# Performance work log

Hardware: AMD Instinct MI355X
Metric: run time of the kernel (lower is better)

The kernel has to match this reference:

```python
import jax, jax.numpy as jnp
import numpy as np

B = 4194304  # batch of 3x3 rotation matrices


def _make_rotations(key, b):
    k1, k2 = jax.random.split(key)
    axis = jax.random.normal(k1, (b, 3), dtype=jnp.float32)
    axis = axis / jnp.linalg.norm(axis, axis=1, keepdims=True)
    # angles bounded away from 0 and pi (s_theta = 2*sin(theta) must be nonzero)
    theta = jax.random.uniform(k2, (b,), dtype=jnp.float32, minval=0.1, maxval=np.pi - 0.1)
    x, y, z = axis[:, 0], axis[:, 1], axis[:, 2]
    zero = jnp.zeros_like(x)
    K = jnp.stack([zero, -z, y, z, zero, -x, -y, x, zero], axis=1).reshape(b, 3, 3)
    I = jnp.eye(3, dtype=jnp.float32)
    s = jnp.sin(theta)[:, None, None]
    c = jnp.cos(theta)[:, None, None]
    return I + s * K + (1.0 - c) * (K @ K)  # Rodrigues


def setup_inputs() -> dict:
    key = jax.random.key(0)
    return {"mat_batch": _make_rotations(key, B)}


def reference(mat_batch) -> jnp.ndarray:
    # rotation angle from trace: theta = acos((tr(R) - 1) / 2)
    tr = jnp.trace(mat_batch, axis1=1, axis2=2)  # [B]
    rot_angle = jnp.arccos((tr - 1.0) / 2.0)[:, None]  # [B,1]
    s_theta = 2.0 * jnp.sin(rot_angle)  # [B,1]
    # unnormalized axis from skew-symmetric part
    w = jnp.stack(
        [
            mat_batch[:, 2, 1] - mat_batch[:, 1, 2],
            mat_batch[:, 0, 2] - mat_batch[:, 2, 0],
            mat_batch[:, 1, 0] - mat_batch[:, 0, 1],
        ],
        axis=1,
    )  # [B,3]
    rot_axis = w / s_theta
    return rot_angle * rot_axis  # [B,3] twist = theta * axis
```

## Files before the change

kernel.cpp:

```cpp
#include <hip/hip_runtime.h>
#include <math.h>


__global__ __launch_bounds__(256) void mat2twist_kernel(
    const float4* __restrict__ in4,
    float4* __restrict__ out4,
    int n_quads,
    const float* __restrict__ in_s,
    float* __restrict__ out_s,
    int n_mat) {

    int idx = blockIdx.x * blockDim.x + threadIdx.x;
    int stride = gridDim.x * blockDim.x;

    for (int q = idx; q < n_quads; q += stride) {
        const float4* p = in4 + (size_t)q * 9;
        float m[36];
#pragma unroll
        for (int i = 0; i < 9; ++i) {
            float4 v = p[i];
            m[4 * i + 0] = v.x;
            m[4 * i + 1] = v.y;
            m[4 * i + 2] = v.z;
            m[4 * i + 3] = v.w;
        }
        float r[12];
#pragma unroll
        for (int j = 0; j < 4; ++j) {
            const float* a = m + 9 * j;
            float tr = a[0] + a[4] + a[8];
            float c  = 0.5f * (tr - 1.0f);
            float ang = acosf(c);
            float s2 = fmaxf(1.0f - c * c, 1e-30f);
            float k  = ang * 0.5f / sqrtf(s2);
            r[3 * j + 0] = k * (a[7] - a[5]);
            r[3 * j + 1] = k * (a[2] - a[6]);
            r[3 * j + 2] = k * (a[3] - a[1]);
        }
        float4* o = out4 + (size_t)q * 3;
        o[0] = make_float4(r[0], r[1], r[2],  r[3]);
        o[1] = make_float4(r[4], r[5], r[6],  r[7]);
        o[2] = make_float4(r[8], r[9], r[10], r[11]);
    }

    if (idx == 0) {
        for (int i = n_quads * 4; i < n_mat; ++i) {
            const float* a = in_s + (size_t)i * 9;
            float tr = a[0] + a[4] + a[8];
            float c  = 0.5f * (tr - 1.0f);
            float ang = acosf(c);
            float s2 = fmaxf(1.0f - c * c, 1e-30f);
            float k  = ang * 0.5f / sqrtf(s2);
            out_s[3 * i + 0] = k * (a[7] - a[5]);
            out_s[3 * i + 1] = k * (a[2] - a[6]);
            out_s[3 * i + 2] = k * (a[3] - a[1]);
        }
    }
}

extern "C" void kernel_launch(void* const* d_in, const int* in_sizes, int n_in,
                              void* d_out, int out_size, void* d_ws, size_t ws_size,
                              hipStream_t stream) {
    const float* in = (const float*)d_in[0];
    float* out = (float*)d_out;
    int n_mat = in_sizes[0] / 9;
    int n_quads = n_mat / 4;

    int block = 256;
    int grid = (n_quads + block - 1) / block;
    if (grid > 4096) grid = 4096;
    if (grid < 1) grid = 1;

    mat2twist_kernel<<<grid, block, 0, stream>>>(
        (const float4*)in, (float4*)out, n_quads, in, out, n_mat);
}
```

Baseline: 223.8 us.

## Stage matrix loads and twist stores through LDS for coalesced global access

Result: no change. 225.5 us (+0.8%).

```diff
diff --git a/kernel.cpp b/kernel.cpp
--- a/kernel.cpp
+++ b/kernel.cpp
@@ -2,7 +2,7 @@
 #include <math.h>
 
 
-__global__ __launch_bounds__(256) void mat2twist_kernel(
+__global__ __launch_bounds__(256) void mat2twist_lds_kernel(
     const float4* __restrict__ in4,
     float4* __restrict__ out4,
     int n_quads,
@@ -10,47 +10,62 @@
     float* __restrict__ out_s,
     int n_mat) {
 
-    int idx = blockIdx.x * blockDim.x + threadIdx.x;
-    int stride = gridDim.x * blockDim.x;
+    __shared__ float4 lds[256 * 9];
 
-    for (int q = idx; q < n_quads; q += stride) {
-        const float4* p = in4 + (size_t)q * 9;
-        float m[36];
+    const int t = threadIdx.x;
+
+    for (int qbase = blockIdx.x * 256; qbase < n_quads; qbase += gridDim.x * 256) {
+        const int quads_here = min(256, n_quads - qbase);
+        const int in_total4  = quads_here * 9;
+
+        const float4* src = in4 + (size_t)qbase * 9;
+        for (int i = t; i < in_total4; i += 256) {
+            lds[i] = src[i];
+        }
+        __syncthreads();
+
+        float r[12];
+        const bool active = t < quads_here;
+        if (active) {
+            const float* m = (const float*)(lds + t * 9);
 #pragma unroll
-        for (int i = 0; i < 9; ++i) {
-            float4 v = p[i];
-            m[4 * i + 0] = v.x;
-            m[4 * i + 1] = v.y;
-            m[4 * i + 2] = v.z;
-            m[4 * i + 3] = v.w;
+            for (int j = 0; j < 4; ++j) {
+                const float* a = m + 9 * j;
+                float tr  = a[0] + a[4] + a[8];
+                float c   = 0.5f * (tr - 1.0f);
+                float ang = acosf(c);
+                float s2  = fmaxf(1.0f - c * c, 1e-30f);
+                float k   = ang * 0.5f / sqrtf(s2);
+                r[3 * j + 0] = k * (a[7] - a[5]);
+                r[3 * j + 1] = k * (a[2] - a[6]);
+                r[3 * j + 2] = k * (a[3] - a[1]);
+            }
         }
-        float r[12];
-#pragma unroll
-        for (int j = 0; j < 4; ++j) {
-            const float* a = m + 9 * j;
-            float tr = a[0] + a[4] + a[8];
-            float c  = 0.5f * (tr - 1.0f);
-            float ang = acosf(c);
-            float s2 = fmaxf(1.0f - c * c, 1e-30f);
-            float k  = ang * 0.5f / sqrtf(s2);
-            r[3 * j + 0] = k * (a[7] - a[5]);
-            r[3 * j + 1] = k * (a[2] - a[6]);
-            r[3 * j + 2] = k * (a[3] - a[1]);
+        __syncthreads();
+
+        if (active) {
+            lds[t * 3 + 0] = make_float4(r[0], r[1], r[2],  r[3]);
+            lds[t * 3 + 1] = make_float4(r[4], r[5], r[6],  r[7]);
+            lds[t * 3 + 2] = make_float4(r[8], r[9], r[10], r[11]);
         }
-        float4* o = out4 + (size_t)q * 3;
-        o[0] = make_float4(r[0], r[1], r[2],  r[3]);
-        o[1] = make_float4(r[4], r[5], r[6],  r[7]);
-        o[2] = make_float4(r[8], r[9], r[10], r[11]);
+        __syncthreads();
+
+        float4* dst = out4 + (size_t)qbase * 3;
+        const int out_total4 = quads_here * 3;
+        for (int i = t; i < out_total4; i += 256) {
+            dst[i] = lds[i];
+        }
+        __syncthreads();
     }
 
-    if (idx == 0) {
+    if (blockIdx.x == 0 && t == 0) {
         for (int i = n_quads * 4; i < n_mat; ++i) {
             const float* a = in_s + (size_t)i * 9;
-            float tr = a[0] + a[4] + a[8];
-            float c  = 0.5f * (tr - 1.0f);
+            float tr  = a[0] + a[4] + a[8];
+            float c   = 0.5f * (tr - 1.0f);
             float ang = acosf(c);
-            float s2 = fmaxf(1.0f - c * c, 1e-30f);
-            float k  = ang * 0.5f / sqrtf(s2);
+            float s2  = fmaxf(1.0f - c * c, 1e-30f);
+            float k   = ang * 0.5f / sqrtf(s2);
             out_s[3 * i + 0] = k * (a[7] - a[5]);
             out_s[3 * i + 1] = k * (a[2] - a[6]);
             out_s[3 * i + 2] = k * (a[3] - a[1]);
@@ -63,14 +78,13 @@
                               hipStream_t stream) {
     const float* in = (const float*)d_in[0];
     float* out = (float*)d_out;
-    int n_mat = in_sizes[0] / 9;
-    int n_quads = n_mat / 4;
+    const int n_mat   = in_sizes[0] / 9;
+    const int n_quads = n_mat / 4;
 
-    int block = 256;
-    int grid = (n_quads + block - 1) / block;
-    if (grid > 4096) grid = 4096;
+    int grid = (n_quads + 255) / 256;
+    if (grid > 8192) grid = 8192;
     if (grid < 1) grid = 1;
 
-    mat2twist_kernel<<<grid, block, 0, stream>>>(
+    mat2twist_lds_kernel<<<grid, 256, 0, stream>>>(
         (const float4*)in, (float4*)out, n_quads, in, out, n_mat);
 }
```
